# Optimization experiments

Measured on AMD Instinct MI355X. Metric: run time of the kernel, lower is better.

## Reference

```python
import jax, jax.numpy as jnp
import numpy as np

B, S, D, H = 2, 2048, 1024, 16
DH = D // H


def setup_inputs() -> dict:
    key = jax.random.key(0)
    ks = jax.random.split(key, 6)
    scale = 1.0 / np.sqrt(D)
    x = jax.random.normal(ks[0], (B, S, D), dtype=jnp.float32)
    mask = jnp.tril(jnp.ones((S, S), dtype=jnp.int32))  # causal 0/1 mask
    Wq = jax.random.normal(ks[1], (D, D), dtype=jnp.float32) * scale
    Wk = jax.random.normal(ks[2], (D, D), dtype=jnp.float32) * scale
    Wv = jax.random.normal(ks[3], (D, D), dtype=jnp.float32) * scale
    Wo = jax.random.normal(ks[4], (D, D), dtype=jnp.float32) * scale
    z = jnp.zeros((D,), dtype=jnp.float32)
    return {"x": x, "mask": mask, "Wq": Wq, "bq": z, "Wk": Wk, "bk": z,
            "Wv": Wv, "bv": z, "Wo": Wo, "bo": z}


def reference(x, mask, Wq, bq, Wk, bk, Wv, bv, Wo, bo):
    # Linear projections (torch Linear: x @ W.T + b; here W stored as [in, out])
    Q = x @ Wq + bq
    K = x @ Wk + bk
    V = x @ Wv + bv
    # [B, S, D] -> [B, H, S, DH]
    Q = Q.reshape(B, S, H, DH).transpose(0, 2, 1, 3)
    K = K.reshape(B, S, H, DH).transpose(0, 2, 1, 3)
    V = V.reshape(B, S, H, DH).transpose(0, 2, 1, 3)
    # scores: [B, H, S, S]
    attn = jnp.einsum('bhqd,bhkd->bhqk', Q, K) / jnp.sqrt(jnp.float32(DH))
    attn = jnp.where(mask == 0, jnp.float32(-1e9), attn)
    scores = jax.nn.softmax(attn, axis=-1)
    # dropout is identity in eval mode
    out = jnp.einsum('bhqk,bhkd->bhqd', scores, V)
    out = out.transpose(0, 2, 1, 3).reshape(B, S, D)
    return out @ Wo + bo
```

## Files before the change

kernel.cpp:

```cpp
#include <hip/hip_runtime.h>
#include <hip/hip_bf16.h>


typedef short bf16x8 __attribute__((ext_vector_type(8)));
typedef float f32x4  __attribute__((ext_vector_type(4)));
typedef short s16x4  __attribute__((ext_vector_type(4)));

#define BB 2
#define SS 2048
#define DD 1024
#define HH 16
#define DHH 64

__device__ __forceinline__ unsigned short f2bf(float f) {
    unsigned u = __builtin_bit_cast(unsigned, f);
    u += 0x7FFFu + ((u >> 16) & 1u);
    return (unsigned short)(u >> 16);
}
__device__ __forceinline__ unsigned short f2bf_trunc(float f) {
    return (unsigned short)(__builtin_bit_cast(unsigned, f) >> 16);
}
__device__ __forceinline__ void cp16(const unsigned short* g, unsigned short* l) {
    __builtin_amdgcn_global_load_lds(
        (const __attribute__((address_space(1))) unsigned int*)(g),
        (__attribute__((address_space(3))) unsigned int*)(l), 16, 0, 0);
}

__global__ __launch_bounds__(256) void prep(
    const float* __restrict__ x,
    const float* __restrict__ w0, const float* __restrict__ w1,
    const float* __restrict__ w2, const float* __restrict__ w3,
    unsigned short* __restrict__ xbf, unsigned short* __restrict__ wt) {
    __shared__ float tile[64][65];
    const int bid = blockIdx.x;
    const int tid = threadIdx.x;
    if (bid < 4096) {
        int i = (bid * 256 + tid) * 4;
        float4 v = *reinterpret_cast<const float4*>(x + i);
        s16x4 p;
        p[0] = (short)f2bf(v.x); p[1] = (short)f2bf(v.y);
        p[2] = (short)f2bf(v.z); p[3] = (short)f2bf(v.w);
        *reinterpret_cast<s16x4*>(xbf + i) = p;
        return;
    }
    const int tb = bid - 4096;
    const int z  = tb >> 8;
    const int bx = (tb & 15) * 64, by = ((tb >> 4) & 15) * 64;
    const float* src = z == 0 ? w0 : z == 1 ? w1 : z == 2 ? w2 : w3;
    unsigned short* out = wt + (size_t)z * (DD * DD);
    const int tx = tid & 63, ty = tid >> 6;
    #pragma unroll
    for (int i = 0; i < 64; i += 4)
        tile[ty + i][tx] = src[(size_t)(by + ty + i) * DD + bx + tx];
    __syncthreads();
    #pragma unroll
    for (int i = 0; i < 64; i += 4)
        out[(size_t)(bx + ty + i) * DD + by + tx] = f2bf(tile[tx][ty + i]);
}

__global__ __launch_bounds__(512, 2) void gemm_qkv(
    const unsigned short* __restrict__ A, const unsigned short* __restrict__ Wt,
    const float* __restrict__ b0, const float* __restrict__ b1,
    const float* __restrict__ b2,
    unsigned short* __restrict__ d0, unsigned short* __restrict__ d1,
    unsigned short* __restrict__ d2) {
    __shared__ __align__(16) unsigned short As_[2][256 * 64];
    __shared__ __align__(16) unsigned short Bs_[2][192 * 64];

    const int tid  = threadIdx.x;
    const int lane = tid & 63;
    const int w    = tid >> 6;
    const int col  = lane & 15;
    const int quad = lane >> 4;
    const int wr   = w >> 2;
    const int wc   = w & 3;
    const int mb   = blockIdx.y * 256;
    const int nb   = blockIdx.x * 192;

    const int r8 = lane >> 3, gg = lane & 7;
    const int srcoff = ((gg ^ r8) * 8);
    const int cswz = col & 7;
    const int pos0 = (quad       ^ cswz) * 8;
    const int pos1 = ((4 + quad) ^ cswz) * 8;

    f32x4 acc[8][3];
    #pragma unroll
    for (int i = 0; i < 8; i++)
        #pragma unroll
        for (int j = 0; j < 3; j++) acc[i][j] = (f32x4){0.f, 0.f, 0.f, 0.f};

    auto stage = [&](int b, int kt) {
        #pragma unroll
        for (int i = 0; i < 4; i++) {
            int rb = w * 32 + i * 8;
            cp16(A + (size_t)(mb + rb + r8) * 1024 + kt + srcoff,
                 As_[b] + rb * 64);
        }
        #pragma unroll
        for (int i = 0; i < 3; i++) {
            int rb = w * 24 + i * 8;
            cp16(Wt + (size_t)(nb + rb + r8) * 1024 + kt + srcoff,
                 Bs_[b] + rb * 64);
        }
    };

    int cur = 0;
    stage(0, 0);
    __syncthreads();

    for (int kt = 0; kt < 1024; kt += 64) {
        if (kt + 64 < 1024) stage(cur ^ 1, kt + 64);
        const unsigned short* Ab = As_[cur];
        const unsigned short* Bb = Bs_[cur];
        #pragma unroll
        for (int p = 0; p < 4; p++) {
            bf16x8 af0[2], af1[2], bq0[3], bq1[3];
            #pragma unroll
            for (int i = 0; i < 2; i++) {
                const unsigned short* ap = Ab + (wr * 128 + p * 32 + i * 16 + col) * 64;
                af0[i] = *reinterpret_cast<const bf16x8*>(ap + pos0);
                af1[i] = *reinterpret_cast<const bf16x8*>(ap + pos1);
            }
            #pragma unroll
            for (int j = 0; j < 3; j++) {
                const unsigned short* bp = Bb + (wc * 48 + j * 16 + col) * 64;
                bq0[j] = *reinterpret_cast<const bf16x8*>(bp + pos0);
                bq1[j] = *reinterpret_cast<const bf16x8*>(bp + pos1);
            }
            __builtin_amdgcn_s_barrier();
            __builtin_amdgcn_s_setprio(1);
            #pragma unroll
            for (int i = 0; i < 2; i++)
                #pragma unroll
                for (int j = 0; j < 3; j++) {
                    acc[p * 2 + i][j] = __builtin_amdgcn_mfma_f32_16x16x32_bf16(
                        af0[i], bq0[j], acc[p * 2 + i][j], 0, 0, 0);
                    acc[p * 2 + i][j] = __builtin_amdgcn_mfma_f32_16x16x32_bf16(
                        af1[i], bq1[j], acc[p * 2 + i][j], 0, 0, 0);
                }
            __builtin_amdgcn_s_setprio(0);
            if (p < 3) __builtin_amdgcn_s_barrier();
        }
        __syncthreads();
        cur ^= 1;
    }

    const float QSCALE = 0.125f * 1.44269504f;
    #pragma unroll
    for (int mi = 0; mi < 8; mi++) {
        int mg = mb + wr * 128 + mi * 16 + quad * 4;
        #pragma unroll
        for (int nj = 0; nj < 3; nj++) {
            int ng = nb + wc * 48 + nj * 16 + col;
            int sel = ng >> 10, n2 = ng & 1023;
            int h = n2 >> 6, dd2 = n2 & 63;
            int b = mg >> 11, s = mg & 2047;
            int bh = b * HH + h;
            const float* bp = sel == 0 ? b0 : sel == 1 ? b1 : b2;
            float bbv = bp[n2];
            if (sel == 0) {
                #pragma unroll
                for (int r = 0; r < 4; r++)
                    d0[((size_t)bh * SS + s + r) * DHH + dd2] = f2bf((acc[mi][nj][r] + bbv) * QSCALE);
            } else if (sel == 1) {
                #pragma unroll
                for (int r = 0; r < 4; r++)
                    d1[((size_t)bh * SS + s + r) * DHH + dd2] = f2bf(acc[mi][nj][r] + bbv);
            } else {
                s16x4 pack;
                #pragma unroll
                for (int r = 0; r < 4; r++) pack[r] = (short)f2bf(acc[mi][nj][r] + bbv);
                *reinterpret_cast<s16x4*>(d2 + ((size_t)bh * DHH + dd2) * SS + s) = pack;
            }
        }
    }
}

__global__ __launch_bounds__(256) void gemm_out(
    const unsigned short* __restrict__ A, const unsigned short* __restrict__ Wt,
    const float* __restrict__ b0, float* __restrict__ d0f) {
    __shared__ __align__(16) unsigned short As[128 * 64];
    __shared__ __align__(16) unsigned short Bs[128 * 64];

    const int tid  = threadIdx.x;
    const int lane = tid & 63;
    const int w    = tid >> 6;
    const int col  = lane & 15;
    const int quad = lane >> 4;
    const int wm   = (w >> 1) * 64;
    const int wn   = (w & 1) * 64;
    const int mb   = blockIdx.y * 128;
    const int nb   = blockIdx.x * 128;

    const int r8 = lane >> 3, gg = lane & 7;
    const int srcoff = ((gg ^ r8) * 8);
    const int cswz = col & 7;

    f32x4 acc[4][4];
    #pragma unroll
    for (int i = 0; i < 4; i++)
        #pragma unroll
        for (int j = 0; j < 4; j++) acc[i][j] = (f32x4){0.f, 0.f, 0.f, 0.f};

    for (int kt = 0; kt < 1024; kt += 64) {
        __syncthreads();
        #pragma unroll
        for (int it = 0; it < 4; it++) {
            int row = w * 32 + it * 8 + r8;
            cp16(A  + (size_t)(mb + row) * 1024 + kt + srcoff, As + (w * 32 + it * 8) * 64);
            cp16(Wt + (size_t)(nb + row) * 1024 + kt + srcoff, Bs + (w * 32 + it * 8) * 64);
        }
        __syncthreads();
        #pragma unroll
        for (int kk = 0; kk < 64; kk += 32) {
            const int kg = (kk >> 3) + quad;
            const int pos = ((kg ^ cswz) * 8);
            bf16x8 af[4], bfr[4];
            #pragma unroll
            for (int i = 0; i < 4; i++)
                af[i] = *reinterpret_cast<const bf16x8*>(As + (wm + i * 16 + col) * 64 + pos);
            #pragma unroll
            for (int j = 0; j < 4; j++)
                bfr[j] = *reinterpret_cast<const bf16x8*>(Bs + (wn + j * 16 + col) * 64 + pos);
            #pragma unroll
            for (int i = 0; i < 4; i++)
                #pragma unroll
                for (int j = 0; j < 4; j++)
                    acc[i][j] = __builtin_amdgcn_mfma_f32_16x16x32_bf16(af[i], bfr[j], acc[i][j], 0, 0, 0);
        }
    }

    #pragma unroll
    for (int i = 0; i < 4; i++) {
        int mg = mb + wm + i * 16 + quad * 4;
        #pragma unroll
        for (int j = 0; j < 4; j++) {
            int ng = nb + wn + j * 16 + col;
            float bbv = b0[ng];
            #pragma unroll
            for (int r = 0; r < 4; r++)
                d0f[(size_t)(mg + r) * 1024 + ng] = acc[i][j][r] + bbv;
        }
    }
}

__global__ __launch_bounds__(256, 4) void attn(
    const unsigned short* __restrict__ Q, const unsigned short* __restrict__ K,
    const unsigned short* __restrict__ Vt, unsigned short* __restrict__ O) {
    __shared__ __align__(16) unsigned short Ks[2][64 * 64];
    __shared__ __align__(16) unsigned short Vs[2][64 * 64];

    const int tid  = threadIdx.x;
    const int lane = tid & 63;
    const int w    = tid >> 6;
    const int col  = lane & 15;
    const int quad = lane >> 4;
    const int bh   = blockIdx.x & 31;
    const int qt   = 31 - (blockIdx.x >> 5);
    const int qb   = qt * 64;
    const int r8 = lane >> 3, gg = lane & 7;
    const int srcoff = ((gg ^ r8) * 8);
    const int cswz = col & 7;
    const int pos0 = (quad       ^ cswz) * 8;
    const int pos1 = ((4 + quad) ^ cswz) * 8;

    bf16x8 onesf;
    #pragma unroll
    for (int j = 0; j < 8; j++) onesf[j] = (col == 0) ? (short)0x3F80 : (short)0;

    const int qrow = qb + w * 16 + col;
    const size_t qbase = ((size_t)bh * SS + qrow) * DHH;
    bf16x8 qlo = *reinterpret_cast<const bf16x8*>(Q + qbase + quad * 8);
    bf16x8 qhi = *reinterpret_cast<const bf16x8*>(Q + qbase + 32 + quad * 8);

    f32x4 o[5];
    #pragma unroll
    for (int d = 0; d < 5; d++) o[d] = (f32x4){0.f, 0.f, 0.f, 0.f};
    float m_i = -1e30f;

    const int ntiles = qt + 1;
    for (int t0 = 0; t0 < ntiles; t0 += 2) {
        const bool two = (t0 + 1 < ntiles);
        __syncthreads();
        #pragma unroll
        for (int it = 0; it < 2; it++) {
            int drow = w * 16 + it * 8;
            int skey = (w >> 1) * 32 + it * 16 + (r8 >> 2) * 8 + (w & 1) * 4 + (r8 & 3);
            cp16(K  + ((size_t)bh * SS + t0 * 64 + skey) * DHH + srcoff,
                 Ks[0] + drow * 64);
            cp16(Vt + ((size_t)bh * DHH + drow + r8) * SS + t0 * 64 + srcoff,
                 Vs[0] + drow * 64);
        }
        if (two) {
            #pragma unroll
            for (int it = 0; it < 2; it++) {
                int drow = w * 16 + it * 8;
                int skey = (w >> 1) * 32 + it * 16 + (r8 >> 2) * 8 + (w & 1) * 4 + (r8 & 3);
                cp16(K  + ((size_t)bh * SS + (t0 + 1) * 64 + skey) * DHH + srcoff,
                     Ks[1] + drow * 64);
                cp16(Vt + ((size_t)bh * DHH + drow + r8) * SS + (t0 + 1) * 64 + srcoff,
                     Vs[1] + drow * 64);
            }
        }
        __syncthreads();

        f32x4 sc[8];
        #pragma unroll
        for (int nt = 0; nt < 4; nt++) {
            int krow = nt * 16 + col;
            bf16x8 klo = *reinterpret_cast<const bf16x8*>(Ks[0] + krow * 64 + pos0);
            bf16x8 khi = *reinterpret_cast<const bf16x8*>(Ks[0] + krow * 64 + pos1);
            f32x4 z = (f32x4){0.f, 0.f, 0.f, 0.f};
            z = __builtin_amdgcn_mfma_f32_16x16x32_bf16(klo, qlo, z, 0, 0, 0);
            z = __builtin_amdgcn_mfma_f32_16x16x32_bf16(khi, qhi, z, 0, 0, 0);
            sc[nt] = z;
        }
        if (two) {
            #pragma unroll
            for (int nt = 0; nt < 4; nt++) {
                int krow = nt * 16 + col;
                bf16x8 klo = *reinterpret_cast<const bf16x8*>(Ks[1] + krow * 64 + pos0);
                bf16x8 khi = *reinterpret_cast<const bf16x8*>(Ks[1] + krow * 64 + pos1);
                f32x4 z = (f32x4){0.f, 0.f, 0.f, 0.f};
                z = __builtin_amdgcn_mfma_f32_16x16x32_bf16(klo, qlo, z, 0, 0, 0);
                z = __builtin_amdgcn_mfma_f32_16x16x32_bf16(khi, qhi, z, 0, 0, 0);
                sc[4 + nt] = z;
            }
        }
        if (t0 == qt || (two && t0 + 1 == qt)) {
            const int sb = (t0 == qt) ? 0 : 4;
            const int tb = (t0 == qt) ? t0 : t0 + 1;
            #pragma unroll
            for (int nt = 0; nt < 4; nt++) {
                #pragma unroll
                for (int r = 0; r < 4; r++) {
                    int kg = tb * 64 + (nt >> 1) * 32 + quad * 8 + (nt & 1) * 4 + r;
                    if (kg > qrow) sc[sb + nt][r] = -3.0e38f;
                }
            }
        }
        float mx = fmaxf(fmaxf(sc[0][0], sc[0][1]), fmaxf(sc[0][2], sc[0][3]));
        #pragma unroll
        for (int nt = 1; nt < 4; nt++)
            mx = fmaxf(mx, fmaxf(fmaxf(sc[nt][0], sc[nt][1]), fmaxf(sc[nt][2], sc[nt][3])));
        if (two) {
            #pragma unroll
            for (int nt = 4; nt < 8; nt++)
                mx = fmaxf(mx, fmaxf(fmaxf(sc[nt][0], sc[nt][1]), fmaxf(sc[nt][2], sc[nt][3])));
        }
        mx = fmaxf(mx, __shfl_xor(mx, 16));
        mx = fmaxf(mx, __shfl_xor(mx, 32));
        float mnew = fmaxf(m_i, mx);
        bool upd = (mnew > m_i);
        if (__any(upd)) {
            float delta = m_i - mnew;
            #pragma unroll
            for (int r = 0; r < 4; r++) {
                float a = exp2f(__shfl(delta, quad * 4 + r));
                #pragma unroll
                for (int d = 0; d < 5; d++) o[d][r] *= a;
            }
        }
        m_i = mnew;

        {
            bf16x8 pf0, pf1;
            #pragma unroll
            for (int j = 0; j < 8; j++) {
                pf0[j] = (short)f2bf_trunc(exp2f(sc[(j >> 2)][j & 3] - mnew));
                pf1[j] = (short)f2bf_trunc(exp2f(sc[2 + (j >> 2)][j & 3] - mnew));
            }
            #pragma unroll
            for (int dt = 0; dt < 4; dt++) {
                int rv = dt * 16 + col;
                bf16x8 vf0 = *reinterpret_cast<const bf16x8*>(Vs[0] + rv * 64 + pos0);
                bf16x8 vf1 = *reinterpret_cast<const bf16x8*>(Vs[0] + rv * 64 + pos1);
                o[dt] = __builtin_amdgcn_mfma_f32_16x16x32_bf16(pf0, vf0, o[dt], 0, 0, 0);
                o[dt] = __builtin_amdgcn_mfma_f32_16x16x32_bf16(pf1, vf1, o[dt], 0, 0, 0);
            }
            o[4] = __builtin_amdgcn_mfma_f32_16x16x32_bf16(pf0, onesf, o[4], 0, 0, 0);
            o[4] = __builtin_amdgcn_mfma_f32_16x16x32_bf16(pf1, onesf, o[4], 0, 0, 0);
        }
        if (two) {
            bf16x8 pf0, pf1;
            #pragma unroll
            for (int j = 0; j < 8; j++) {
                pf0[j] = (short)f2bf_trunc(exp2f(sc[4 + (j >> 2)][j & 3] - mnew));
                pf1[j] = (short)f2bf_trunc(exp2f(sc[6 + (j >> 2)][j & 3] - mnew));
            }
            #pragma unroll
            for (int dt = 0; dt < 4; dt++) {
                int rv = dt * 16 + col;
                bf16x8 vf0 = *reinterpret_cast<const bf16x8*>(Vs[1] + rv * 64 + pos0);
                bf16x8 vf1 = *reinterpret_cast<const bf16x8*>(Vs[1] + rv * 64 + pos1);
                o[dt] = __builtin_amdgcn_mfma_f32_16x16x32_bf16(pf0, vf0, o[dt], 0, 0, 0);
                o[dt] = __builtin_amdgcn_mfma_f32_16x16x32_bf16(pf1, vf1, o[dt], 0, 0, 0);
            }
            o[4] = __builtin_amdgcn_mfma_f32_16x16x32_bf16(pf0, onesf, o[4], 0, 0, 0);
            o[4] = __builtin_amdgcn_mfma_f32_16x16x32_bf16(pf1, onesf, o[4], 0, 0, 0);
        }
    }

    #pragma unroll
    for (int r = 0; r < 4; r++) {
        float lv = __shfl(o[4][r], lane & 48);
        float inv = 1.0f / lv;
        int sq = qb + w * 16 + quad * 4 + r;
        size_t base = ((size_t)(bh >> 4) * SS + sq) * DD + (size_t)(bh & 15) * DHH;
        #pragma unroll
        for (int dt = 0; dt < 4; dt++)
            O[base + dt * 16 + col] = f2bf(o[dt][r] * inv);
    }
}

extern "C" void kernel_launch(void* const* d_in, const int* in_sizes, int n_in,
                              void* d_out, int out_size, void* d_ws, size_t ws_size,
                              hipStream_t stream) {
    (void)in_sizes; (void)n_in; (void)out_size; (void)ws_size;
    const float* x  = (const float*)d_in[0];
    const float* Wq = (const float*)d_in[2];
    const float* bq = (const float*)d_in[3];
    const float* Wk = (const float*)d_in[4];
    const float* bk = (const float*)d_in[5];
    const float* Wv = (const float*)d_in[6];
    const float* bv = (const float*)d_in[7];
    const float* Wo = (const float*)d_in[8];
    const float* bo = (const float*)d_in[9];
    float* out = (float*)d_out;

    char* ws = (char*)d_ws;
    unsigned short* xbf = (unsigned short*)(ws);
    unsigned short* qws = (unsigned short*)(ws + ((size_t)8  << 20));
    unsigned short* kws = (unsigned short*)(ws + ((size_t)16 << 20));
    unsigned short* vws = (unsigned short*)(ws + ((size_t)24 << 20));
    unsigned short* wt  = (unsigned short*)(ws + ((size_t)32 << 20));
    unsigned short* ows = xbf;

    prep<<<dim3(5120), 256, 0, stream>>>(x, Wq, Wk, Wv, Wo, xbf, wt);
    gemm_qkv<<<dim3(16, 16), 512, 0, stream>>>(xbf, wt, bq, bk, bv,
                                               qws, kws, vws);
    attn<<<dim3(1024), 256, 0, stream>>>(qws, kws, vws, ows);
    gemm_out<<<dim3(8, 32), 256, 0, stream>>>(ows, wt + (size_t)3 * 1024 * 1024,
                                              bo, out);
}
```

Measured before the change: 205.4 us.

## Double-buffer output GEMM, swizzle block order, simplify QKV GEMM inner loop

The output projection GEMM now double-buffers its LDS tiles, prefetching the next K tile while computing the current one. Before, it loaded and computed serially with two barriers per step. Both GEMMs remap block indices with an XCD-style swizzle so neighbouring tiles land on the same die for L2 reuse. The QKV GEMM drops its per-subtile s_barrier/setprio ping-pong in favour of loading the B fragments once per K step and streaming A rows. The gemm_out LDS footprint doubles, and removing the barrier scheduling may change how waves interleave.

```diff
diff --git a/kernel.cpp b/kernel.cpp
--- a/kernel.cpp
+++ b/kernel.cpp
@@ -74,8 +74,11 @@
     const int quad = lane >> 4;
     const int wr   = w >> 2;
     const int wc   = w & 3;
-    const int mb   = blockIdx.y * 256;
-    const int nb   = blockIdx.x * 192;
+
+    const int flat = blockIdx.y * 16 + blockIdx.x;
+    const int swz  = (flat & 7) * 32 + (flat >> 3);
+    const int mb   = (swz >> 4) * 256;
+    const int nb   = (swz & 15) * 192;
 
     const int r8 = lane >> 3, gg = lane & 7;
     const int srcoff = ((gg ^ r8) * 8);
@@ -112,34 +115,23 @@
         if (kt + 64 < 1024) stage(cur ^ 1, kt + 64);
         const unsigned short* Ab = As_[cur];
         const unsigned short* Bb = Bs_[cur];
-        #pragma unroll
-        for (int p = 0; p < 4; p++) {
-            bf16x8 af0[2], af1[2], bq0[3], bq1[3];
-            #pragma unroll
-            for (int i = 0; i < 2; i++) {
-                const unsigned short* ap = Ab + (wr * 128 + p * 32 + i * 16 + col) * 64;
-                af0[i] = *reinterpret_cast<const bf16x8*>(ap + pos0);
-                af1[i] = *reinterpret_cast<const bf16x8*>(ap + pos1);
-            }
+        bf16x8 bq0[3], bq1[3];
+        #pragma unroll
+        for (int j = 0; j < 3; j++) {
+            const unsigned short* bp = Bb + (wc * 48 + j * 16 + col) * 64;
+            bq0[j] = *reinterpret_cast<const bf16x8*>(bp + pos0);
+            bq1[j] = *reinterpret_cast<const bf16x8*>(bp + pos1);
+        }
+        #pragma unroll
+        for (int mi = 0; mi < 8; mi++) {
+            const unsigned short* ap = Ab + (wr * 128 + mi * 16 + col) * 64;
+            bf16x8 a0 = *reinterpret_cast<const bf16x8*>(ap + pos0);
+            bf16x8 a1 = *reinterpret_cast<const bf16x8*>(ap + pos1);
             #pragma unroll
             for (int j = 0; j < 3; j++) {
-                const unsigned short* bp = Bb + (wc * 48 + j * 16 + col) * 64;
-                bq0[j] = *reinterpret_cast<const bf16x8*>(bp + pos0);
-                bq1[j] = *reinterpret_cast<const bf16x8*>(bp + pos1);
-            }
-            __builtin_amdgcn_s_barrier();
-            __builtin_amdgcn_s_setprio(1);
-            #pragma unroll
-            for (int i = 0; i < 2; i++)
-                #pragma unroll
-                for (int j = 0; j < 3; j++) {
-                    acc[p * 2 + i][j] = __builtin_amdgcn_mfma_f32_16x16x32_bf16(
-                        af0[i], bq0[j], acc[p * 2 + i][j], 0, 0, 0);
-                    acc[p * 2 + i][j] = __builtin_amdgcn_mfma_f32_16x16x32_bf16(
-                        af1[i], bq1[j], acc[p * 2 + i][j], 0, 0, 0);
-                }
-            __builtin_amdgcn_s_setprio(0);
-            if (p < 3) __builtin_amdgcn_s_barrier();
+                acc[mi][j] = __builtin_amdgcn_mfma_f32_16x16x32_bf16(a0, bq0[j], acc[mi][j], 0, 0, 0);
+                acc[mi][j] = __builtin_amdgcn_mfma_f32_16x16x32_bf16(a1, bq1[j], acc[mi][j], 0, 0, 0);
+            }
         }
         __syncthreads();
         cur ^= 1;
@@ -179,8 +171,8 @@
 __global__ __launch_bounds__(256) void gemm_out(
     const unsigned short* __restrict__ A, const unsigned short* __restrict__ Wt,
     const float* __restrict__ b0, float* __restrict__ d0f) {
-    __shared__ __align__(16) unsigned short As[128 * 64];
-    __shared__ __align__(16) unsigned short Bs[128 * 64];
+    __shared__ __align__(16) unsigned short As_[2][128 * 64];
+    __shared__ __align__(16) unsigned short Bs_[2][128 * 64];
 
     const int tid  = threadIdx.x;
     const int lane = tid & 63;
@@ -189,12 +181,17 @@
     const int quad = lane >> 4;
     const int wm   = (w >> 1) * 64;
     const int wn   = (w & 1) * 64;
-    const int mb   = blockIdx.y * 128;
-    const int nb   = blockIdx.x * 128;
+
+    const int flat = blockIdx.y * 8 + blockIdx.x;
+    const int swz  = (flat & 7) * 32 + (flat >> 3);
+    const int mb   = (swz >> 3) * 128;
+    const int nb   = (swz & 7) * 128;
 
     const int r8 = lane >> 3, gg = lane & 7;
     const int srcoff = ((gg ^ r8) * 8);
     const int cswz = col & 7;
+    const int pos0 = (quad       ^ cswz) * 8;
+    const int pos1 = ((4 + quad) ^ cswz) * 8;
 
     f32x4 acc[4][4];
     #pragma unroll
@@ -202,32 +199,43 @@
         #pragma unroll
         for (int j = 0; j < 4; j++) acc[i][j] = (f32x4){0.f, 0.f, 0.f, 0.f};
 
+    auto stage = [&](int b, int kt) {
+        #pragma unroll
+        for (int it = 0; it < 4; it++) {
+            int row = w * 32 + it * 8;
+            cp16(A  + (size_t)(mb + row + r8) * 1024 + kt + srcoff, As_[b] + row * 64);
+            cp16(Wt + (size_t)(nb + row + r8) * 1024 + kt + srcoff, Bs_[b] + row * 64);
+        }
+    };
+
+    int cur = 0;
+    stage(0, 0);
+    __syncthreads();
+
     for (int kt = 0; kt < 1024; kt += 64) {
+        if (kt + 64 < 1024) stage(cur ^ 1, kt + 64);
+        const unsigned short* Ab = As_[cur];
+        const unsigned short* Bb = Bs_[cur];
+        bf16x8 bq0[4], bq1[4];
+        #pragma unroll
+        for (int j = 0; j < 4; j++) {
+            const unsigned short* bp = Bb + (wn + j * 16 + col) * 64;
+            bq0[j] = *reinterpret_cast<const bf16x8*>(bp + pos0);
+            bq1[j] = *reinterpret_cast<const bf16x8*>(bp + pos1);
+        }
+        #pragma unroll
+        for (int i = 0; i < 4; i++) {
+            const unsigned short* ap = Ab + (wm + i * 16 + col) * 64;
+            bf16x8 a0 = *reinterpret_cast<const bf16x8*>(ap + pos0);
+            bf16x8 a1 = *reinterpret_cast<const bf16x8*>(ap + pos1);
+            #pragma unroll
+            for (int j = 0; j < 4; j++) {
+                acc[i][j] = __builtin_amdgcn_mfma_f32_16x16x32_bf16(a0, bq0[j], acc[i][j], 0, 0, 0);
+                acc[i][j] = __builtin_amdgcn_mfma_f32_16x16x32_bf16(a1, bq1[j], acc[i][j], 0, 0, 0);
+            }
+        }
         __syncthreads();
-        #pragma unroll
-        for (int it = 0; it < 4; it++) {
-            int row = w * 32 + it * 8 + r8;
-            cp16(A  + (size_t)(mb + row) * 1024 + kt + srcoff, As + (w * 32 + it * 8) * 64);
-            cp16(Wt + (size_t)(nb + row) * 1024 + kt + srcoff, Bs + (w * 32 + it * 8) * 64);
-        }
-        __syncthreads();
-        #pragma unroll
-        for (int kk = 0; kk < 64; kk += 32) {
-            const int kg = (kk >> 3) + quad;
-            const int pos = ((kg ^ cswz) * 8);
-            bf16x8 af[4], bfr[4];
-            #pragma unroll
-            for (int i = 0; i < 4; i++)
-                af[i] = *reinterpret_cast<const bf16x8*>(As + (wm + i * 16 + col) * 64 + pos);
-            #pragma unroll
-            for (int j = 0; j < 4; j++)
-                bfr[j] = *reinterpret_cast<const bf16x8*>(Bs + (wn + j * 16 + col) * 64 + pos);
-            #pragma unroll
-            for (int i = 0; i < 4; i++)
-                #pragma unroll
-                for (int j = 0; j < 4; j++)
-                    acc[i][j] = __builtin_amdgcn_mfma_f32_16x16x32_bf16(af[i], bfr[j], acc[i][j], 0, 0, 0);
-        }
+        cur ^= 1;
     }
 
     #pragma unroll
```

Measured after the change: 190.2 us. -7.4%, faster.
